# Kernel tuning notes

Hardware: AMD Instinct MI355X
Metric: run time of the kernel (lower is better)

## Reference

```python
import jax, jax.numpy as jnp
import numpy as np

NUM_HEADS = 12
HEAD_DIM = 64
NPT = 1  # num_prefix_tokens

def _rot(x):
    # pairs (x0,x1) -> (-x1, x0), matching timm's rot()
    x2 = x.reshape(*x.shape[:-1], -1, 2)
    r = jnp.stack([-x2[..., 1], x2[..., 0]], axis=-1)
    return r.reshape(x.shape)

def _apply_rope_cat(x, rope):
    # rope: [N_rot, 2*hd] = sin||cos concatenated
    sin, cos = jnp.split(rope, 2, axis=-1)
    return x * cos + _rot(x) * sin

def setup_inputs() -> dict:
    key = jax.random.key(0)
    ks = jax.random.split(key, 7)
    B, N, C = 8, 4097, 768
    hd = HEAD_DIM
    x = jax.random.normal(ks[0], (B, N, C), jnp.float32)
    rope = jax.random.normal(ks[1], (N - NPT, 2 * hd), jnp.float32)
    qkv_w = jax.random.normal(ks[2], (3 * C, C), jnp.float32) * (C ** -0.5)
    q_bias = jax.random.normal(ks[3], (C,), jnp.float32) * 0.02
    v_bias = jax.random.normal(ks[4], (C,), jnp.float32) * 0.02
    proj_w = jax.random.normal(ks[5], (C, C), jnp.float32) * (C ** -0.5)
    proj_b = jax.random.normal(ks[6], (C,), jnp.float32) * 0.02
    return dict(x=x, rope=rope, qkv_w=qkv_w, q_bias=q_bias, v_bias=v_bias,
                proj_w=proj_w, proj_b=proj_b)

def reference(x, rope, qkv_w, q_bias, v_bias, proj_w, proj_b):
    B, N, C = x.shape
    H, hd = NUM_HEADS, HEAD_DIM
    # fused QKV with k_bias fixed at zero (non-trainable buffer)
    bias = jnp.concatenate([q_bias, jnp.zeros_like(q_bias), v_bias])
    qkv = x @ qkv_w.T + bias                            # [B,N,3C]
    qkv = qkv.reshape(B, N, 3, H, hd).transpose(2, 0, 3, 1, 4)
    q, k, v = qkv[0], qkv[1], qkv[2]                    # [B,H,N,hd]
    # RoPE on all tokens except the prefix (CLS) token
    q = jnp.concatenate([q[:, :, :NPT], _apply_rope_cat(q[:, :, NPT:], rope)], axis=2)
    k = jnp.concatenate([k[:, :, :NPT], _apply_rope_cat(k[:, :, NPT:], rope)], axis=2)
    # linear attention: kv = K^T V, then Q @ kv, normalized by hd*N
    kv = jnp.einsum('bhnd,bhne->bhde', k, v)            # [B,H,hd,hd]
    out = jnp.einsum('bhnd,bhde->bhne', q, kv) / hd / N # [B,H,N,hd]
    out = out.transpose(0, 2, 1, 3).reshape(B, N, C)
    return out @ proj_w.T + proj_b
```

## Files before the change

### kernel.cpp

```cpp
#include <hip/hip_runtime.h>
#include <hip/hip_bf16.h>

typedef __attribute__((ext_vector_type(8))) short short8;
typedef __attribute__((ext_vector_type(4))) short short4v;
typedef __attribute__((ext_vector_type(4))) float f32x4;

#define B_    8
#define N_    4097
#define C_    768
#define M_TOT (B_*N_)
#define K3    (3*C_)
#define CHUNKS 16
#define NSTEP 24

__device__ __forceinline__ float bf2f(unsigned short u) {
  union { unsigned int i; float f; } x; x.i = ((unsigned int)u) << 16; return x.f;
}
__device__ __forceinline__ unsigned short f2bf(float f) {
  union { float f; unsigned int i; } x; x.f = f;
  unsigned int i = x.i + 0x7fffu + ((x.i >> 16) & 1u);
  return (unsigned short)(i >> 16);
}
__device__ __forceinline__ void gload16(const void* g, void* l) {
  __builtin_amdgcn_global_load_lds(
      (const __attribute__((address_space(1))) void*)g,
      (__attribute__((address_space(3))) void*)l, 16, 0, 0);
}

__global__ __launch_bounds__(256) void cvt_kernel(const float* __restrict__ inx,
                                                  unsigned short* __restrict__ outx,
                                                  const float* __restrict__ inw,
                                                  unsigned short* __restrict__ outw,
                                                  long n4x, long n4tot) {
  long i = (long)blockIdx.x * blockDim.x + threadIdx.x;
  long stride = (long)gridDim.x * blockDim.x;
  for (; i < n4tot; i += stride) {
    const float4* src; ushort4* dst; long j;
    if (i < n4x) { src = (const float4*)inx; dst = (ushort4*)outx; j = i; }
    else         { src = (const float4*)inw; dst = (ushort4*)outw; j = i - n4x; }
    float4 v = src[j];
    ushort4 o;
    o.x = f2bf(v.x); o.y = f2bf(v.y); o.z = f2bf(v.z); o.w = f2bf(v.w);
    dst[j] = o;
  }
}

__global__ __launch_bounds__(512, 4) void gemm_qkv_rope(
    const unsigned short* __restrict__ A,
    const unsigned short* __restrict__ Bw,
    const float* __restrict__ rope,
    const float* __restrict__ qb,
    const float* __restrict__ vb,
    unsigned short* __restrict__ qkv)
{
  __shared__ __align__(16) char L[3*24576];
  const int tid  = threadIdx.x;
  const int wave = tid >> 6, lane = tid & 63;
  const int lr = lane & 15, lk = lane >> 4;
  const int wm = wave >> 2, wn = wave & 3;

  const int o = blockIdx.x;
  const int xcd = o & 7, loc = o >> 3;
  const int tile = (xcd < 1 ? xcd*290 : 290 + (xcd-1)*289) + loc;
  const int m0 = (tile / 9) * 128;
  const int n0 = (tile % 9) * 256;

  const int arow = tid >> 2, achk = tid & 3;
  const int am = min(m0 + arow, M_TOT-1);
  const unsigned short* gA  = A  + (long)am*768 + achk*8;
  const unsigned short* gB1 = Bw + (long)(n0 + arow)*768 + achk*8;
  const unsigned short* gB2 = Bw + (long)(n0 + arow + 128)*768 + achk*8;
  const int dA  = wave*1024;
  const int dB1 = 8192  + wave*1024;
  const int dB2 = 16384 + wave*1024;

  const int abase = (wm*64 + lr)*64 + lk*16;
  const int bbase = 8192 + (wn*64 + lr)*64 + lk*16;

  f32x4 acc[4][4];
#pragma unroll
  for (int i = 0; i < 4; ++i)
#pragma unroll
    for (int j = 0; j < 4; ++j) acc[i][j] = (f32x4){0.f,0.f,0.f,0.f};

  auto STAGE = [&](int buf, int kk) {
    char* sb = L + buf*24576;
    gload16(gA  + kk, sb + dA);
    gload16(gB1 + kk, sb + dB1);
    gload16(gB2 + kk, sb + dB2);
  };
  auto COMPUTE = [&](int buf) {
    const char* sb = L + buf*24576;
    short8 af[4], bfr[4];
#pragma unroll
    for (int mi = 0; mi < 4; ++mi)
      af[mi] = *(const short8*)(sb + abase + mi*1024);
#pragma unroll
    for (int ni = 0; ni < 4; ++ni)
      bfr[ni] = *(const short8*)(sb + bbase + ni*1024);
#pragma unroll
    for (int mi = 0; mi < 4; ++mi)
#pragma unroll
      for (int ni = 0; ni < 4; ++ni)
        acc[mi][ni] = __builtin_amdgcn_mfma_f32_16x16x32_bf16(af[mi], bfr[ni], acc[mi][ni], 0, 0, 0);
  };

  STAGE(0, 0);
  STAGE(1, 32);
  asm volatile("s_waitcnt vmcnt(3)" ::: "memory");
  __builtin_amdgcn_s_barrier();
  __builtin_amdgcn_sched_barrier(0);

  int cur = 0;
  for (int tt = 0; tt < NSTEP-2; ++tt) {
    int stg = cur + 2; if (stg >= 3) stg -= 3;
    STAGE(stg, (tt+2)*32);
    COMPUTE(cur);
    asm volatile("s_waitcnt vmcnt(3)" ::: "memory");
    __builtin_amdgcn_sched_barrier(0);
    __builtin_amdgcn_s_barrier();
    __builtin_amdgcn_sched_barrier(0);
    cur = (cur + 1 == 3) ? 0 : cur + 1;
  }
  COMPUTE(cur);
  asm volatile("s_waitcnt vmcnt(0)" ::: "memory");
  __builtin_amdgcn_sched_barrier(0);
  __builtin_amdgcn_s_barrier();
  __builtin_amdgcn_sched_barrier(0);
  cur = (cur + 1 == 3) ? 0 : cur + 1;
  COMPUTE(cur);

  const int which = n0 / 768;
  unsigned short* plane = qkv + (long)which*M_TOT*768;

  float biasv[4]; int withv[4]; int dv[4];
#pragma unroll
  for (int ni = 0; ni < 4; ++ni) {
    const int gc = n0 + wn*64 + ni*16 + lr;
    const int within = gc - which*768;
    withv[ni] = within;
    dv[ni] = within & 63;
    biasv[ni] = (which == 0) ? qb[within] : (which == 2 ? vb[within] : 0.f);
  }

  if (which == 2) {
#pragma unroll
    for (int mi = 0; mi < 4; ++mi)
#pragma unroll
      for (int r = 0; r < 4; ++r) {
        const int gm = m0 + wm*64 + mi*16 + lk*4 + r;
        if (gm < M_TOT) {
#pragma unroll
          for (int ni = 0; ni < 4; ++ni)
            plane[(long)gm*768 + withv[ni]] = f2bf(acc[mi][ni][r] + biasv[ni]);
        }
      }
  } else {
#pragma unroll
    for (int mi = 0; mi < 4; ++mi) {
#pragma unroll
      for (int r = 0; r < 4; ++r) {
        const int gm = m0 + wm*64 + mi*16 + lk*4 + r;
        const int ntok = gm % 4097;
        const bool valid = gm < M_TOT;
        const bool dorope = (ntok > 0) && valid;
        const float* rp = rope + (long)(ntok - 1)*128;
#pragma unroll
        for (int ni = 0; ni < 4; ++ni) {
          float v = acc[mi][ni][r] + biasv[ni];
          float pair = __shfl_xor(v, 1);
          float vo = v;
          if (dorope) {
            const float s = rp[dv[ni]], c = rp[64 + dv[ni]];
            const float rot = (dv[ni] & 1) ? pair : -pair;
            vo = v*c + rot*s;
          }
          if (valid) plane[(long)gm*768 + withv[ni]] = f2bf(vo);
        }
      }
    }
  }
}

__global__ __launch_bounds__(256) void kv_partial_kernel(
    const unsigned short* __restrict__ qkv, float* __restrict__ part)
{
  const int bh = blockIdx.y;
  const int b = bh / 12, h = bh % 12;
  const int chunk = blockIdx.x;
  const int per = (N_ + CHUNKS - 1) / CHUNKS;
  const int nst = chunk * per;
  const int nen = min(nst + per, N_);
  const unsigned short* Kpl = qkv + (long)M_TOT*768 + ((long)b*N_)*768 + h*64;
  const unsigned short* Vpl = qkv + (long)2*M_TOT*768 + ((long)b*N_)*768 + h*64;

  __shared__ __align__(16) unsigned short Kt[2][2048];
  __shared__ __align__(16) unsigned short Vt[2][2048];

  const int t = threadIdx.x;
  const int lrow = t >> 3, lpc = t & 7;
  const int wave = t >> 6, lane = t & 63;
  const int soff = ((lpc >> 1)*8 + (lrow >> 2))*64 + (lrow & 3)*16 + (lpc & 1)*8;

  f32x4 acc[4];
#pragma unroll
  for (int e = 0; e < 4; ++e) acc[e] = (f32x4){0.f,0.f,0.f,0.f};

  {
    const int cnt0 = min(32, nen - nst);
    uint4 k0 = {0,0,0,0}, v0 = {0,0,0,0};
    if (lrow < cnt0) {
      k0 = *(const uint4*)(Kpl + (long)(nst + lrow)*768 + lpc*8);
      v0 = *(const uint4*)(Vpl + (long)(nst + lrow)*768 + lpc*8);
    }
    *(uint4*)(Kt[0] + soff) = k0;
    *(uint4*)(Vt[0] + soff) = v0;
  }

  int cur = 0;
  for (int nb = nst; nb < nen; nb += 32) {
    uint4 kn = {0,0,0,0}, vn = {0,0,0,0};
    const int nxt = nb + 32;
    if (nxt < nen) {
      const int cntn = min(32, nen - nxt);
      if (lrow < cntn) {
        kn = *(const uint4*)(Kpl + (long)(nxt + lrow)*768 + lpc*8);
        vn = *(const uint4*)(Vpl + (long)(nxt + lrow)*768 + lpc*8);
      }
    }
    __syncthreads();

    {
      const unsigned short* kb = Kt[cur] + wave*512;
      const unsigned short* vb_ = Vt[cur];
      short4v a0, a1;
      const unsigned short* ka = kb + lane*4;
      asm volatile("ds_read_b64_tr_b16 %0, %1" : "=v"(a0)
                   : "v"((unsigned)(__builtin_amdgcn_is_shared((const __attribute__((address_space(0))) void*)ka), (unsigned)(unsigned long)(ka - (const unsigned short*)0))));
      (void)a0; (void)a1;
    }
    {
      short4v ak0, ak1, bv0[4], bv1[4];
      unsigned kaddr = (unsigned)(unsigned long)(uintptr_t)(Kt[cur] + wave*512 + lane*4);
      asm volatile("ds_read_b64_tr_b16 %0, %1"            : "=v"(ak0) : "v"(kaddr));
      asm volatile("ds_read_b64_tr_b16 %0, %1 offset:512" : "=v"(ak1) : "v"(kaddr));
#pragma unroll
      for (int eblk = 0; eblk < 4; ++eblk) {
        unsigned vaddr = (unsigned)(unsigned long)(uintptr_t)(Vt[cur] + eblk*512 + lane*4);
        asm volatile("ds_read_b64_tr_b16 %0, %1"            : "=v"(bv0[eblk]) : "v"(vaddr));
        asm volatile("ds_read_b64_tr_b16 %0, %1 offset:512" : "=v"(bv1[eblk]) : "v"(vaddr));
      }
      asm volatile("s_waitcnt lgkmcnt(0)" ::: "memory");
      __builtin_amdgcn_sched_barrier(0);
      short8 afr;
      afr[0]=ak0[0]; afr[1]=ak0[1]; afr[2]=ak0[2]; afr[3]=ak0[3];
      afr[4]=ak1[0]; afr[5]=ak1[1]; afr[6]=ak1[2]; afr[7]=ak1[3];
#pragma unroll
      for (int eblk = 0; eblk < 4; ++eblk) {
        short8 bfr;
        bfr[0]=bv0[eblk][0]; bfr[1]=bv0[eblk][1]; bfr[2]=bv0[eblk][2]; bfr[3]=bv0[eblk][3];
        bfr[4]=bv1[eblk][0]; bfr[5]=bv1[eblk][1]; bfr[6]=bv1[eblk][2]; bfr[7]=bv1[eblk][3];
        acc[eblk] = __builtin_amdgcn_mfma_f32_16x16x32_bf16(afr, bfr, acc[eblk], 0, 0, 0);
      }
    }
    __syncthreads();
    if (nxt < nen) {
      *(uint4*)(Kt[cur^1] + soff) = kn;
      *(uint4*)(Vt[cur^1] + soff) = vn;
    }
    cur ^= 1;
  }

  float* base = part + ((long)chunk*96 + bh)*4096;
  const int d0 = wave*16 + (lane >> 4)*4;
  const int e0 = lane & 15;
#pragma unroll
  for (int eblk = 0; eblk < 4; ++eblk)
#pragma unroll
    for (int r = 0; r < 4; ++r)
      base[(long)(d0 + r)*64 + eblk*16 + e0] = acc[eblk][r];
}

__global__ __launch_bounds__(256) void mcomb_kernel(const float* __restrict__ part,
                                                    const float* __restrict__ pw,
                                                    unsigned short* __restrict__ McT) {
  const int blk = blockIdx.x;
  const int cs = blk & 3;
  const int h  = (blk >> 2) % 12;
  const int b  = blk / 48;
  const int bh = b*12 + h;
  __shared__ float kvs[64][65];
  const int t = threadIdx.x;
  const int d_own = t >> 2;
  const int eg = (t & 3) * 16;

  float4 a0 = {0,0,0,0}, a1 = {0,0,0,0}, a2 = {0,0,0,0}, a3 = {0,0,0,0};
  const float4* p4 = (const float4*)part;
#pragma unroll
  for (int ch = 0; ch < CHUNKS; ++ch) {
    const long base = ((long)ch*96 + bh)*1024 + d_own*16 + (t & 3)*4;
    float4 v0 = p4[base+0], v1 = p4[base+1], v2 = p4[base+2], v3 = p4[base+3];
    a0.x += v0.x; a0.y += v0.y; a0.z += v0.z; a0.w += v0.w;
    a1.x += v1.x; a1.y += v1.y; a1.z += v1.z; a1.w += v1.w;
    a2.x += v2.x; a2.y += v2.y; a2.z += v2.z; a2.w += v2.w;
    a3.x += v3.x; a3.y += v3.y; a3.z += v3.z; a3.w += v3.w;
  }
  kvs[eg+ 0][d_own] = a0.x; kvs[eg+ 1][d_own] = a0.y; kvs[eg+ 2][d_own] = a0.z; kvs[eg+ 3][d_own] = a0.w;
  kvs[eg+ 4][d_own] = a1.x; kvs[eg+ 5][d_own] = a1.y; kvs[eg+ 6][d_own] = a1.z; kvs[eg+ 7][d_own] = a1.w;
  kvs[eg+ 8][d_own] = a2.x; kvs[eg+ 9][d_own] = a2.y; kvs[eg+10][d_own] = a2.z; kvs[eg+11][d_own] = a2.w;
  kvs[eg+12][d_own] = a3.x; kvs[eg+13][d_own] = a3.y; kvs[eg+14][d_own] = a3.z; kvs[eg+15][d_own] = a3.w;
  __syncthreads();

  const int lane = t & 63;
  const int w    = t >> 6;
  float kvcol[64];
#pragma unroll
  for (int e = 0; e < 64; ++e) kvcol[e] = kvs[e][lane];

  const float scale = (float)(1.0/(64.0*4097.0));
  const int cbase = cs*192 + w*48;
  for (int i = 0; i < 48; ++i) {
    const int c = cbase + i;
    const float* pwrow = pw + (long)c*768 + h*64;
    float s = 0.f;
#pragma unroll
    for (int e = 0; e < 64; ++e) s += pwrow[e] * kvcol[e];
    McT[((long)b*768 + c)*768 + h*64 + lane] = f2bf(s * scale);
  }
}

__global__ __launch_bounds__(512, 4) void gemm_final(
    const unsigned short* __restrict__ qkv,
    const unsigned short* __restrict__ McT,
    const float* __restrict__ pb,
    float* __restrict__ out)
{
  __shared__ __align__(16) char L[3*24576];
  const int tid  = threadIdx.x;
  const int wave = tid >> 6, lane = tid & 63;
  const int lr = lane & 15, lk = lane >> 4;
  const int wm = wave >> 2, wn = wave & 3;

  const int o = blockIdx.x;
  const int xcd = o & 7, loc = o >> 3;
  const int b  = xcd;
  const int mt = loc / 3, ct = loc % 3;
  const int m0 = mt * 128;
  const int c0 = ct * 256;

  const int arow = tid >> 2, achk = tid & 3;
  const int am = min(m0 + arow, N_-1);
  const unsigned short* gA  = qkv + ((long)b*N_ + am)*768 + achk*8;
  const unsigned short* Bb  = McT + (long)b*768*768;
  const unsigned short* gB1 = Bb + (long)(c0 + arow)*768 + achk*8;
  const unsigned short* gB2 = Bb + (long)(c0 + arow + 128)*768 + achk*8;
  const int dA  = wave*1024;
  const int dB1 = 8192  + wave*1024;
  const int dB2 = 16384 + wave*1024;

  const int abase = (wm*64 + lr)*64 + lk*16;
  const int bbase = 8192 + (wn*64 + lr)*64 + lk*16;

  f32x4 acc[4][4];
#pragma unroll
  for (int i = 0; i < 4; ++i)
#pragma unroll
    for (int j = 0; j < 4; ++j) acc[i][j] = (f32x4){0.f,0.f,0.f,0.f};

  auto STAGE = [&](int buf, int kk) {
    char* sb = L + buf*24576;
    gload16(gA  + kk, sb + dA);
    gload16(gB1 + kk, sb + dB1);
    gload16(gB2 + kk, sb + dB2);
  };
  auto COMPUTE = [&](int buf) {
    const char* sb = L + buf*24576;
    short8 af[4], bfr[4];
#pragma unroll
    for (int mi = 0; mi < 4; ++mi)
      af[mi] = *(const short8*)(sb + abase + mi*1024);
#pragma unroll
    for (int ni = 0; ni < 4; ++ni)
      bfr[ni] = *(const short8*)(sb + bbase + ni*1024);
#pragma unroll
    for (int mi = 0; mi < 4; ++mi)
#pragma unroll
      for (int ni = 0; ni < 4; ++ni)
        acc[mi][ni] = __builtin_amdgcn_mfma_f32_16x16x32_bf16(af[mi], bfr[ni], acc[mi][ni], 0, 0, 0);
  };

  STAGE(0, 0);
  STAGE(1, 32);
  asm volatile("s_waitcnt vmcnt(3)" ::: "memory");
  __builtin_amdgcn_s_barrier();
  __builtin_amdgcn_sched_barrier(0);

  int cur = 0;
  for (int tt = 0; tt < NSTEP-2; ++tt) {
    int stg = cur + 2; if (stg >= 3) stg -= 3;
    STAGE(stg, (tt+2)*32);
    COMPUTE(cur);
    asm volatile("s_waitcnt vmcnt(3)" ::: "memory");
    __builtin_amdgcn_sched_barrier(0);
    __builtin_amdgcn_s_barrier();
    __builtin_amdgcn_sched_barrier(0);
    cur = (cur + 1 == 3) ? 0 : cur + 1;
  }
  COMPUTE(cur);
  asm volatile("s_waitcnt vmcnt(0)" ::: "memory");
  __builtin_amdgcn_sched_barrier(0);
  __builtin_amdgcn_s_barrier();
  __builtin_amdgcn_sched_barrier(0);
  cur = (cur + 1 == 3) ? 0 : cur + 1;
  COMPUTE(cur);

#pragma unroll
  for (int mi = 0; mi < 4; ++mi) {
#pragma unroll
    for (int ni = 0; ni < 4; ++ni) {
      const int gc = c0 + wn*64 + ni*16 + lr;
      const float bias = pb[gc];
#pragma unroll
      for (int r = 0; r < 4; ++r) {
        const int tok = m0 + wm*64 + mi*16 + lk*4 + r;
        if (tok < N_)
          out[((long)b*N_ + tok)*768 + gc] = acc[mi][ni][r] + bias;
      }
    }
  }
}

extern "C" void kernel_launch(void* const* d_in, const int* in_sizes, int n_in,
                              void* d_out, int out_size, void* d_ws, size_t ws_size,
                              hipStream_t stream) {
  const float* x      = (const float*)d_in[0];
  const float* rope   = (const float*)d_in[1];
  const float* qkv_w  = (const float*)d_in[2];
  const float* q_bias = (const float*)d_in[3];
  const float* v_bias = (const float*)d_in[4];
  const float* proj_w = (const float*)d_in[5];
  const float* proj_b = (const float*)d_in[6];
  float* out = (float*)d_out;

  char* w0 = (char*)d_ws;
  unsigned short* x_bf  = (unsigned short*)w0;
  unsigned short* wq_bf = (unsigned short*)(w0 + 50343936);
  unsigned short* qkv   = (unsigned short*)(w0 + 50343936 + 3538944);
  float*          part  = (float*)w0;
  unsigned short* McT   = (unsigned short*)(w0 + 25165824 + 1572864);

  const long n4x = (long)M_TOT*768/4;
  const long n4w = (long)K3*768/4;
  cvt_kernel<<<2048, 256, 0, stream>>>(x, x_bf, qkv_w, wq_bf, n4x, n4x + n4w);

  gemm_qkv_rope<<<2313, 512, 0, stream>>>(x_bf, wq_bf, rope, q_bias, v_bias, qkv);

  kv_partial_kernel<<<dim3(CHUNKS, 96), 256, 0, stream>>>(qkv, part);
  mcomb_kernel<<<384, 256, 0, stream>>>(part, proj_w, McT);

  gemm_final<<<792, 512, 0, stream>>>(qkv, McT, proj_b, out);
}
```

Measured before the change: 355.9 us.

## Fuse fp32-to-bf16 conversion of x into QKV GEMM A-tile staging

Removes the separate pass that converted the large activation tensor x to bf16. The QKV GEMM now loads fp32 x directly through registers, converts it to bf16 and writes it into LDS one stage ahead, while the weight tiles keep using async global-to-LDS loads. The standalone convert kernel now handles only the weights, and the workspace layout is reorganised. A dead transposed LDS read in the kv partial kernel is also dropped. The trade is that the GEMM reads twice the A bytes per tile, uses more registers and does extra VALU conversion work, but it avoids writing and re-reading about 50MB of bf16 x.

```diff
diff --git a/kernel.cpp b/kernel.cpp
--- a/kernel.cpp
+++ b/kernel.cpp
@@ -27,26 +27,21 @@
       (__attribute__((address_space(3))) void*)l, 16, 0, 0);
 }
 
-__global__ __launch_bounds__(256) void cvt_kernel(const float* __restrict__ inx,
-                                                  unsigned short* __restrict__ outx,
-                                                  const float* __restrict__ inw,
-                                                  unsigned short* __restrict__ outw,
-                                                  long n4x, long n4tot) {
+__global__ __launch_bounds__(256) void cvt_kernel(const float* __restrict__ in,
+                                                  unsigned short* __restrict__ out,
+                                                  long n4) {
   long i = (long)blockIdx.x * blockDim.x + threadIdx.x;
   long stride = (long)gridDim.x * blockDim.x;
-  for (; i < n4tot; i += stride) {
-    const float4* src; ushort4* dst; long j;
-    if (i < n4x) { src = (const float4*)inx; dst = (ushort4*)outx; j = i; }
-    else         { src = (const float4*)inw; dst = (ushort4*)outw; j = i - n4x; }
-    float4 v = src[j];
+  for (; i < n4; i += stride) {
+    float4 v = ((const float4*)in)[i];
     ushort4 o;
     o.x = f2bf(v.x); o.y = f2bf(v.y); o.z = f2bf(v.z); o.w = f2bf(v.w);
-    dst[j] = o;
+    ((ushort4*)out)[i] = o;
   }
 }
 
 __global__ __launch_bounds__(512, 4) void gemm_qkv_rope(
-    const unsigned short* __restrict__ A,
+    const float* __restrict__ X,
     const unsigned short* __restrict__ Bw,
     const float* __restrict__ rope,
     const float* __restrict__ qb,
@@ -67,12 +62,12 @@
 
   const int arow = tid >> 2, achk = tid & 3;
   const int am = min(m0 + arow, M_TOT-1);
-  const unsigned short* gA  = A  + (long)am*768 + achk*8;
+  const float*          gX  = X  + (long)am*768 + achk*8;
   const unsigned short* gB1 = Bw + (long)(n0 + arow)*768 + achk*8;
   const unsigned short* gB2 = Bw + (long)(n0 + arow + 128)*768 + achk*8;
-  const int dA  = wave*1024;
   const int dB1 = 8192  + wave*1024;
   const int dB2 = 16384 + wave*1024;
+  const int dAw = wave*1024 + lane*16;
 
   const int abase = (wm*64 + lr)*64 + lk*16;
   const int bbase = 8192 + (wn*64 + lr)*64 + lk*16;
@@ -83,11 +78,16 @@
 #pragma unroll
     for (int j = 0; j < 4; ++j) acc[i][j] = (f32x4){0.f,0.f,0.f,0.f};
 
-  auto STAGE = [&](int buf, int kk) {
+  auto STAGE_B = [&](int buf, int kk) {
     char* sb = L + buf*24576;
-    gload16(gA  + kk, sb + dA);
     gload16(gB1 + kk, sb + dB1);
     gload16(gB2 + kk, sb + dB2);
+  };
+  auto WRITE_A = [&](int buf, const float4& fa, const float4& fb) {
+    short8 v;
+    v[0]=(short)f2bf(fa.x); v[1]=(short)f2bf(fa.y); v[2]=(short)f2bf(fa.z); v[3]=(short)f2bf(fa.w);
+    v[4]=(short)f2bf(fb.x); v[5]=(short)f2bf(fb.y); v[6]=(short)f2bf(fb.z); v[7]=(short)f2bf(fb.w);
+    *(short8*)(L + buf*24576 + dAw) = v;
   };
   auto COMPUTE = [&](int buf) {
     const char* sb = L + buf*24576;
@@ -105,29 +105,56 @@
         acc[mi][ni] = __builtin_amdgcn_mfma_f32_16x16x32_bf16(af[mi], bfr[ni], acc[mi][ni], 0, 0, 0);
   };
 
-  STAGE(0, 0);
-  STAGE(1, 32);
-  asm volatile("s_waitcnt vmcnt(3)" ::: "memory");
-  __builtin_amdgcn_s_barrier();
-  __builtin_amdgcn_sched_barrier(0);
+  float4 pa0, pa1;
+  {
+    float4 a00 = *(const float4*)(gX + 0);
+    float4 a01 = *(const float4*)(gX + 4);
+    __builtin_amdgcn_sched_barrier(0);
+    STAGE_B(0, 0);
+    __builtin_amdgcn_sched_barrier(0);
+    pa0 = *(const float4*)(gX + 32);
+    pa1 = *(const float4*)(gX + 36);
+    __builtin_amdgcn_sched_barrier(0);
+    STAGE_B(1, 32);
+    __builtin_amdgcn_sched_barrier(0);
+    WRITE_A(0, a00, a01);
+    asm volatile("s_waitcnt vmcnt(4)" ::: "memory");
+    asm volatile("s_waitcnt lgkmcnt(0)" ::: "memory");
+    __builtin_amdgcn_s_barrier();
+    __builtin_amdgcn_sched_barrier(0);
+  }
 
   int cur = 0;
   for (int tt = 0; tt < NSTEP-2; ++tt) {
     int stg = cur + 2; if (stg >= 3) stg -= 3;
-    STAGE(stg, (tt+2)*32);
+    int wsl = cur + 1; if (wsl >= 3) wsl -= 3;
+    const int kk = (tt+2)*32;
+    float4 na0 = *(const float4*)(gX + kk);
+    float4 na1 = *(const float4*)(gX + kk + 4);
+    __builtin_amdgcn_sched_barrier(0);
+    STAGE_B(stg, kk);
+    __builtin_amdgcn_sched_barrier(0);
     COMPUTE(cur);
-    asm volatile("s_waitcnt vmcnt(3)" ::: "memory");
-    __builtin_amdgcn_sched_barrier(0);
+    asm volatile("s_waitcnt vmcnt(4)" ::: "memory");
+    __builtin_amdgcn_sched_barrier(0);
+    WRITE_A(wsl, pa0, pa1);
+    asm volatile("s_waitcnt lgkmcnt(0)" ::: "memory");
     __builtin_amdgcn_s_barrier();
     __builtin_amdgcn_sched_barrier(0);
+    pa0 = na0; pa1 = na1;
     cur = (cur + 1 == 3) ? 0 : cur + 1;
   }
-  COMPUTE(cur);
-  asm volatile("s_waitcnt vmcnt(0)" ::: "memory");
-  __builtin_amdgcn_sched_barrier(0);
-  __builtin_amdgcn_s_barrier();
-  __builtin_amdgcn_sched_barrier(0);
-  cur = (cur + 1 == 3) ? 0 : cur + 1;
+  {
+    int wsl = cur + 1; if (wsl >= 3) wsl -= 3;
+    COMPUTE(cur);
+    asm volatile("s_waitcnt vmcnt(0)" ::: "memory");
+    __builtin_amdgcn_sched_barrier(0);
+    WRITE_A(wsl, pa0, pa1);
+    asm volatile("s_waitcnt lgkmcnt(0)" ::: "memory");
+    __builtin_amdgcn_s_barrier();
+    __builtin_amdgcn_sched_barrier(0);
+    cur = (cur + 1 == 3) ? 0 : cur + 1;
+  }
   COMPUTE(cur);
 
   const int which = n0 / 768;
@@ -230,15 +257,6 @@
     }
     __syncthreads();
 
-    {
-      const unsigned short* kb = Kt[cur] + wave*512;
-      const unsigned short* vb_ = Vt[cur];
-      short4v a0, a1;
-      const unsigned short* ka = kb + lane*4;
-      asm volatile("ds_read_b64_tr_b16 %0, %1" : "=v"(a0)
-                   : "v"((unsigned)(__builtin_amdgcn_is_shared((const __attribute__((address_space(0))) void*)ka), (unsigned)(unsigned long)(ka - (const unsigned short*)0))));
-      (void)a0; (void)a1;
-    }
     {
       short4v ak0, ak1, bv0[4], bv1[4];
       unsigned kaddr = (unsigned)(unsigned long)(uintptr_t)(Kt[cur] + wave*512 + lane*4);
@@ -443,17 +461,14 @@
   float* out = (float*)d_out;
 
   char* w0 = (char*)d_ws;
-  unsigned short* x_bf  = (unsigned short*)w0;
-  unsigned short* wq_bf = (unsigned short*)(w0 + 50343936);
-  unsigned short* qkv   = (unsigned short*)(w0 + 50343936 + 3538944);
-  float*          part  = (float*)w0;
-  unsigned short* McT   = (unsigned short*)(w0 + 25165824 + 1572864);
-
-  const long n4x = (long)M_TOT*768/4;
-  const long n4w = (long)K3*768/4;
-  cvt_kernel<<<2048, 256, 0, stream>>>(x, x_bf, qkv_w, wq_bf, n4x, n4x + n4w);
-
-  gemm_qkv_rope<<<2313, 512, 0, stream>>>(x_bf, wq_bf, rope, q_bias, v_bias, qkv);
+  unsigned short* wq_bf = (unsigned short*)w0;
+  float*          part  = (float*)(w0 + 4194304);
+  unsigned short* McT   = (unsigned short*)(w0 + 29360128);
+  unsigned short* qkv   = (unsigned short*)(w0 + 41943040);
+
+  cvt_kernel<<<432, 256, 0, stream>>>(qkv_w, wq_bf, (long)K3*768/4);
+
+  gemm_qkv_rope<<<2313, 512, 0, stream>>>(x, wq_bf, rope, q_bias, v_bias, qkv);
 
   kv_partial_kernel<<<dim3(CHUNKS, 96), 256, 0, stream>>>(qkv, part);
   mcomb_kernel<<<384, 256, 0, stream>>>(part, proj_w, McT);
```

After: 376.0 us. 5.6% more time.
